# Kernel tuning notes

Measured on AMD Instinct MI355X. Metric: run time of the kernel, lower is better.

Reference implementation:

```python
import jax, jax.numpy as jnp
import numpy as np

B, T, D = 8, 1024, 1024
H, HD, KVH, R = 16, 64, 4, 256   # heads, head_dim, kv_heads, kv_lora_rank
K = 31                            # depthwise conv kernel
FF = 4 * D
EPS = 1e-5


def _ln(x, g, b):
    m = jnp.mean(x, -1, keepdims=True)
    v = jnp.mean((x - m) ** 2, -1, keepdims=True)
    return (x - m) * jax.lax.rsqrt(v + EPS) * g + b


def _rope_tables(seq, dim):
    inv = 1.0 / (10000.0 ** (np.arange(0, dim, 2, dtype=np.float32) / dim))
    t = np.arange(seq, dtype=np.float32)
    f = np.einsum('i,j->ij', t, inv)
    emb = np.concatenate([f, f], -1)
    return jnp.asarray(np.cos(emb)), jnp.asarray(np.sin(emb))


def _rope(x, cos, sin):
    # x: [B, h, T, HD]; cos/sin: [T, HD]
    x1, x2 = jnp.split(x, 2, axis=-1)
    return x * cos + jnp.concatenate([-x2, x1], -1) * sin


def setup_inputs() -> dict:
    key = jax.random.key(0)
    ks = iter(jax.random.split(key, 48))
    def w(shape, s=0.02):
        return jax.random.normal(next(ks), shape, jnp.float32) * s
    d = {}
    d['x'] = jax.random.normal(next(ks), (B, T, D), jnp.float32)
    d['ff1_ng'] = jnp.ones(D); d['ff1_nb'] = jnp.zeros(D)
    d['ff1_w1'] = w((D, FF)); d['ff1_b1'] = jnp.zeros(FF)
    d['ff1_w2'] = w((FF, D)); d['ff1_b2'] = jnp.zeros(D)
    d['attn_ng'] = jnp.ones(D); d['attn_nb'] = jnp.zeros(D)
    d['wq'] = w((D, H * HD)); d['wkva'] = w((D, R + HD))
    d['kvn_g'] = jnp.ones(R); d['kvn_b'] = jnp.zeros(R)
    d['wkvb'] = w((R, KVH * HD * 2)); d['wo'] = w((H * HD, D))
    d['conv_ng'] = jnp.ones(D); d['conv_nb'] = jnp.zeros(D)
    d['pw1_w'] = w((D, 2 * D)); d['pw1_b'] = jnp.zeros(2 * D)
    d['dw_w'] = w((D, 1, K)); d['dw_b'] = jnp.zeros(D)
    d['bn_g'] = jnp.ones(D); d['bn_b'] = jnp.zeros(D)
    d['bn_rm'] = jnp.zeros(D); d['bn_rv'] = jnp.ones(D)
    d['pw2_w'] = w((D, D)); d['pw2_b'] = jnp.zeros(D)
    d['ff2_ng'] = jnp.ones(D); d['ff2_nb'] = jnp.zeros(D)
    d['ff2_w1'] = w((D, FF)); d['ff2_b1'] = jnp.zeros(FF)
    d['ff2_w2'] = w((FF, D)); d['ff2_b2'] = jnp.zeros(D)
    d['fin_g'] = jnp.ones(D); d['fin_b'] = jnp.zeros(D)
    return d


def _ffn(x, ng, nb, w1, b1, w2, b2):
    h = jax.nn.silu(_ln(x, ng, nb) @ w1 + b1)
    return h @ w2 + b2


def _rmla(x, ng, nb, wq, wkva, kvn_g, kvn_b, wkvb, wo):
    h = _ln(x, ng, nb)
    q = (h @ wq).reshape(B, T, H, HD).transpose(0, 2, 1, 3)
    kva = h @ wkva                                  # [B,T,R+HD]; k_pe part unused (as in source)
    lat = _ln(kva[..., :R], kvn_g, kvn_b)
    kv = lat @ wkvb
    k = kv[..., :KVH * HD].reshape(B, T, KVH, HD).transpose(0, 2, 1, 3)
    v = kv[..., KVH * HD:].reshape(B, T, KVH, HD).transpose(0, 2, 1, 3)
    cos, sin = _rope_tables(T, HD)
    q = _rope(q, cos, sin)
    k = _rope(k, cos, sin)
    g = H // KVH
    k = jnp.repeat(k, g, axis=1)
    v = jnp.repeat(v, g, axis=1)
    s = jnp.einsum('bhqd,bhkd->bhqk', q, k) * (HD ** -0.5)
    a = jax.nn.softmax(s.astype(jnp.float32), axis=-1).astype(q.dtype)
    o = jnp.einsum('bhqk,bhkd->bhqd', a, v)
    o = o.transpose(0, 2, 1, 3).reshape(B, T, H * HD)
    return o @ wo


def _convmod(x, ng, nb, pw1_w, pw1_b, dw_w, dw_b, bn_g, bn_b, bn_rm, bn_rv, pw2_w, pw2_b):
    h = _ln(x, ng, nb)
    h = h @ pw1_w + pw1_b                           # [B,T,2D]
    a, gate = jnp.split(h, 2, axis=-1)
    h = a * jax.nn.sigmoid(gate)                    # GLU over channels
    h = h.transpose(0, 2, 1)                        # [B,D,T]
    h = jax.lax.conv_general_dilated(h, dw_w, (1,), [(K // 2, K // 2)],
                                     dimension_numbers=('NCH', 'OIH', 'NCH'),
                                     feature_group_count=D) + dw_b[None, :, None]
    h = (h - bn_rm[None, :, None]) * jax.lax.rsqrt(bn_rv[None, :, None] + EPS)
    h = h * bn_g[None, :, None] + bn_b[None, :, None]
    h = jax.nn.silu(h)
    h = h.transpose(0, 2, 1)                        # [B,T,D]
    return h @ pw2_w + pw2_b


def reference(x, ff1_ng, ff1_nb, ff1_w1, ff1_b1, ff1_w2, ff1_b2,
              attn_ng, attn_nb, wq, wkva, kvn_g, kvn_b, wkvb, wo,
              conv_ng, conv_nb, pw1_w, pw1_b, dw_w, dw_b, bn_g, bn_b, bn_rm, bn_rv, pw2_w, pw2_b,
              ff2_ng, ff2_nb, ff2_w1, ff2_b1, ff2_w2, ff2_b2, fin_g, fin_b):
    # Conformer block (macaron): half-FF, RMLA attention, gated depthwise conv, half-FF, final LN
    x = x + 0.5 * _ffn(x, ff1_ng, ff1_nb, ff1_w1, ff1_b1, ff1_w2, ff1_b2)
    x = x + _rmla(x, attn_ng, attn_nb, wq, wkva, kvn_g, kvn_b, wkvb, wo)
    x = x + _convmod(x, conv_ng, conv_nb, pw1_w, pw1_b, dw_w, dw_b, bn_g, bn_b, bn_rm, bn_rv, pw2_w, pw2_b)
    x = x + 0.5 * _ffn(x, ff2_ng, ff2_nb, ff2_w1, ff2_b1, ff2_w2, ff2_b2)
    return _ln(x, fin_g, fin_b)
```

## Files before the change

### kernel.cpp

```cpp
#include <hip/hip_runtime.h>
#include <stdint.h>

typedef unsigned short u16;
using bf16x8 = __attribute__((ext_vector_type(8))) __bf16;
using f32x4  = __attribute__((ext_vector_type(4))) float;

__device__ __forceinline__ u16 f2bf(float f) {
    uint32_t u = __float_as_uint(f);
    u += 0x7fffu + ((u >> 16) & 1u);
    return (u16)(u >> 16);
}
__device__ __forceinline__ float bf2f(u16 u) {
    return __uint_as_float(((uint32_t)u) << 16);
}
__device__ __forceinline__ void gload16(const void* g, void* l) {
    __builtin_amdgcn_global_load_lds(
        (__attribute__((address_space(1))) void*)(uintptr_t)g,
        (__attribute__((address_space(3))) void*)(uintptr_t)l,
        16, 0, 0);
}

template <int OUTF32>
__global__ __launch_bounds__(256) void ln_kernel(const float* __restrict__ in,
                                                 const float* __restrict__ g,
                                                 const float* __restrict__ b,
                                                 void* __restrict__ out, int D) {
    const int row = blockIdx.x;
    const int tid = threadIdx.x;
    const float* x = in + (size_t)row * D;
    const int nv = D >> 8;
    float v[4];
    float s1 = 0.f, s2 = 0.f;
    for (int i = 0; i < nv; ++i) {
        float t = x[tid + (i << 8)];
        v[i] = t; s1 += t; s2 += t * t;
    }
    for (int o = 1; o < 64; o <<= 1) {
        s1 += __shfl_xor(s1, o, 64);
        s2 += __shfl_xor(s2, o, 64);
    }
    __shared__ float r1[4], r2[4];
    const int w = tid >> 6;
    if ((tid & 63) == 0) { r1[w] = s1; r2[w] = s2; }
    __syncthreads();
    s1 = r1[0] + r1[1] + r1[2] + r1[3];
    s2 = r2[0] + r2[1] + r2[2] + r2[3];
    const float mean = s1 / (float)D;
    const float var  = s2 / (float)D - mean * mean;
    const float inv  = rsqrtf(var + 1e-5f);
    for (int i = 0; i < nv; ++i) {
        int c = tid + (i << 8);
        float y = (v[i] - mean) * inv * g[c] + b[c];
        if (OUTF32) ((float*)out)[(size_t)row * D + c] = y;
        else        ((u16*)out)[(size_t)row * D + c] = f2bf(y);
    }
}

template <int GLUPERM>
__global__ __launch_bounds__(256) void wconvert_t(const float* __restrict__ W,
                                                  u16* __restrict__ Wt,
                                                  int K, int N, int ldw) {
    __shared__ float tile[32][33];
    const int k0 = blockIdx.x * 32, n0 = blockIdx.y * 32;
    const int tx = threadIdx.x & 31, ty = threadIdx.x >> 5;
    const int csrc = GLUPERM ? ((tx & 1) * 1024 + (n0 >> 1) + (tx >> 1)) : (n0 + tx);
    for (int i = 0; i < 4; ++i)
        tile[ty + i * 8][tx] = W[(size_t)(k0 + ty + i * 8) * ldw + csrc];
    __syncthreads();
    for (int i = 0; i < 4; ++i)
        Wt[(size_t)(n0 + ty + i * 8) * K + k0 + tx] = f2bf(tile[tx][ty + i * 8]);
}

template <int EPI>
__global__ __launch_bounds__(256) void gemm_bf16(const u16* __restrict__ A,
                                                 const u16* __restrict__ Bt,
                                                 const float* __restrict__ bias,
                                                 const float* __restrict__ res,
                                                 float rscale,
                                                 void* __restrict__ outp,
                                                 int M, int N, int K, int nbx) {
    __shared__ u16 sA[128 * 64];
    __shared__ u16 sB[128 * 64];
    const int tid = threadIdx.x;
    const int lane = tid & 63;
    const int w = tid >> 6;
    const int wm = w >> 1, wn = w & 1;
    const int fr = lane & 15, fq = lane >> 4, frx = fr & 7;
    const int cpx = gridDim.x >> 3;
    const int lid = (blockIdx.x & 7) * cpx + (blockIdx.x >> 3);
    const int bn0 = (lid % nbx) * 128;
    const int bm0 = (lid / nbx) * 128;

    f32x4 acc[4][4] = {};

    const int lrow = lane >> 3;
    const int lslot = (lane & 7) ^ lrow;
    const u16* ga0 = A  + (size_t)(bm0 + w * 8 + lrow) * K + lslot * 8;
    const u16* gb0 = Bt + (size_t)(bn0 + w * 8 + lrow) * K + lslot * 8;
    u16* la0 = sA + w * 512;
    u16* lb0 = sB + w * 512;
    const size_t rstep32 = (size_t)32 * K;

    for (int kt = 0; kt < K; kt += 64) {
        __syncthreads();
#pragma unroll
        for (int i = 0; i < 4; ++i) {
            gload16(ga0 + kt + i * rstep32, la0 + i * 2048);
            gload16(gb0 + kt + i * rstep32, lb0 + i * 2048);
        }
        __syncthreads();
#pragma unroll
        for (int kk = 0; kk < 2; ++kk) {
            bf16x8 afr[4], bfr[4];
            const int sl = (((kk * 4 + fq) ^ frx) << 3);
#pragma unroll
            for (int i = 0; i < 4; ++i) {
                afr[i] = *(const bf16x8*)(sA + (wm * 64 + i * 16 + fr) * 64 + sl);
                bfr[i] = *(const bf16x8*)(sB + (wn * 64 + i * 16 + fr) * 64 + sl);
            }
#pragma unroll
            for (int mi = 0; mi < 4; ++mi)
#pragma unroll
                for (int ni = 0; ni < 4; ++ni)
                    acc[mi][ni] = __builtin_amdgcn_mfma_f32_16x16x32_bf16(
                        bfr[ni], afr[mi], acc[mi][ni], 0, 0, 0);
        }
    }

#pragma unroll
    for (int mi = 0; mi < 4; ++mi) {
        const int m = bm0 + wm * 64 + mi * 16 + fr;
#pragma unroll
        for (int ni = 0; ni < 4; ++ni) {
            const int n0 = bn0 + wn * 64 + ni * 16 + fq * 4;
            if (EPI == 0 || EPI == 1) {
                union { uint2 u2; u16 hh[4]; } ok;
#pragma unroll
                for (int r = 0; r < 4; ++r) {
                    float v = acc[mi][ni][r] + (bias ? bias[n0 + r] : 0.f);
                    if (EPI == 1) v = v / (1.f + __expf(-v));
                    ok.hh[r] = f2bf(v);
                }
                *(uint2*)((u16*)outp + (size_t)m * N + n0) = ok.u2;
            } else if (EPI == 2) {
                f32x4 v;
#pragma unroll
                for (int r = 0; r < 4; ++r)
                    v[r] = acc[mi][ni][r] + (bias ? bias[n0 + r] : 0.f);
                *(f32x4*)((float*)outp + (size_t)m * N + n0) = v;
            } else if (EPI == 3) {
                const f32x4 rv = *(const f32x4*)(res + (size_t)m * N + n0);
                f32x4 v;
#pragma unroll
                for (int r = 0; r < 4; ++r)
                    v[r] = rv[r] + rscale * (acc[mi][ni][r] + (bias ? bias[n0 + r] : 0.f));
                *(f32x4*)((float*)outp + (size_t)m * N + n0) = v;
            } else {
                float vv[4];
#pragma unroll
                for (int r = 0; r < 4; ++r) {
                    const int n = n0 + r;
                    vv[r] = acc[mi][ni][r] + bias[((n & 1) << 10) + (n >> 1)];
                }
                union { uint32_t u; u16 hh[2]; } ok;
                ok.hh[0] = f2bf(vv[0] / (1.f + __expf(-vv[1])));
                ok.hh[1] = f2bf(vv[2] / (1.f + __expf(-vv[3])));
                *(uint32_t*)((u16*)outp + (size_t)m * (N >> 1) + (n0 >> 1)) = ok.u;
            }
        }
    }
}

__global__ __launch_bounds__(256) void rope_tables_kernel(float* __restrict__ ct,
                                                          float* __restrict__ st) {
    const int i = blockIdx.x * 256 + threadIdx.x;
    const int t = i >> 5, j = i & 31;
    const float inv = powf(10000.f, -(float)j / 32.f);
    const float f = (float)t * inv;
    ct[i] = cosf(f);
    st[i] = sinf(f);
}

__global__ __launch_bounds__(256) void rope_kernel(u16* __restrict__ buf,
                                                   const float* __restrict__ ct,
                                                   const float* __restrict__ st,
                                                   int hmask, int hshift, int rstride,
                                                   float scale) {
    const int i = blockIdx.x * 256 + threadIdx.x;
    const int j = i & 31;
    const int hh = (i >> 5) & hmask;
    const int m = i >> (5 + hshift);
    const int t = m & 1023;
    u16* p = buf + (size_t)m * rstride + hh * 64 + j;
    const float c = ct[t * 32 + j], s = st[t * 32 + j];
    const float x1 = bf2f(p[0]), x2 = bf2f(p[32]);
    p[0]  = f2bf((x1 * c - x2 * s) * scale);
    p[32] = f2bf((x2 * c + x1 * s) * scale);
}

__global__ __launch_bounds__(256) void vtranspose_kernel(const u16* __restrict__ KV,
                                                         u16* __restrict__ Vt) {
    __shared__ u16 tile[32][33];
    const int t0 = blockIdx.x * 32, h0 = blockIdx.y * 32;
    const int bk = blockIdx.z;
    const int b = bk >> 2, kh = bk & 3;
    const int tx = threadIdx.x & 31, ty = threadIdx.x >> 5;
    for (int i = 0; i < 4; ++i)
        tile[ty + i * 8][tx] =
            KV[(size_t)(b * 1024 + t0 + ty + i * 8) * 512 + 256 + kh * 64 + h0 + tx];
    __syncthreads();
    for (int i = 0; i < 4; ++i)
        Vt[((size_t)bk * 64 + h0 + ty + i * 8) * 1024 + t0 + tx] = tile[tx][ty + i * 8];
}

__global__ __launch_bounds__(256) void attn_kernel(const u16* __restrict__ Q,
                                                   const u16* __restrict__ KV,
                                                   const u16* __restrict__ Vt,
                                                   u16* __restrict__ O) {
    __shared__ __align__(16) u16 sK[2][64 * 64];
    __shared__ __align__(16) u16 sV[2][64 * 64];
    __shared__ __align__(16) u16 sP[4][16 * 64];
    const int tid = threadIdx.x, lane = tid & 63, w = tid >> 6;
    const int fr = lane & 15, fq = lane >> 4, frx = fr & 7;
    const int bk = blockIdx.x, b = bk >> 2, kh = bk & 3;
    const int h = kh * 4 + w;
    const int q0 = blockIdx.y * 16;
    const int qrow = b * 1024 + q0 + fr;

    const int srow = w * 16 + (lane >> 3);
    const int sslot = (lane & 7) ^ ((lane >> 3) & 7);
    const u16* gK = KV + (size_t)(b * 1024 + srow) * 512 + kh * 64 + sslot * 8;
    const u16* gV = Vt + (size_t)((b * 4 + kh) * 64 + srow) * 1024 + sslot * 8;
    u16* dK = (u16*)sK + w * 16 * 64;
    u16* dV = (u16*)sV + w * 16 * 64;

    bf16x8 qf[2];
    qf[0] = *(const bf16x8*)(Q + (size_t)qrow * 1024 + h * 64 + fq * 8);
    qf[1] = *(const bf16x8*)(Q + (size_t)qrow * 1024 + h * 64 + 32 + fq * 8);

    f32x4 oacc[4] = {};
    float mrun = -1e30f, lrun = 0.f;
    u16* sPw = sP[w];

    gload16(gK, dK);
    gload16(gK + (size_t)8 * 512, dK + 8 * 64);
    gload16(gV, dV);
    gload16(gV + (size_t)8 * 1024, dV + 8 * 64);
    __syncthreads();

    int cur = 0;
    for (int t = 0; t < 16; ++t) {
        const int kv0 = t * 64;
        if (t < 15) {
            const int kn = kv0 + 64;
            const int nx = (cur ^ 1) * 4096;
            gload16(gK + (size_t)kn * 512,       dK + nx);
            gload16(gK + (size_t)(kn + 8) * 512, dK + nx + 8 * 64);
            gload16(gV + kn,                     dV + nx);
            gload16(gV + kn + (size_t)8 * 1024,  dV + nx + 8 * 64);
        }
        const u16* sKc = (u16*)sK + cur * 4096;
        const u16* sVc = (u16*)sV + cur * 4096;
        f32x4 sacc[4] = {};
#pragma unroll
        for (int ks = 0; ks < 2; ++ks)
#pragma unroll
            for (int nb = 0; nb < 4; ++nb) {
                const bf16x8 kf = *(const bf16x8*)(
                    sKc + (nb * 16 + fr) * 64 + (((ks * 4 + fq) ^ frx) << 3));
                sacc[nb] = __builtin_amdgcn_mfma_f32_16x16x32_bf16(kf, qf[ks], sacc[nb], 0, 0, 0);
            }
        float pm;
        {
            float a0 = fmaxf(fmaxf(sacc[0][0], sacc[0][1]), fmaxf(sacc[0][2], sacc[0][3]));
            float a1 = fmaxf(fmaxf(sacc[1][0], sacc[1][1]), fmaxf(sacc[1][2], sacc[1][3]));
            float a2 = fmaxf(fmaxf(sacc[2][0], sacc[2][1]), fmaxf(sacc[2][2], sacc[2][3]));
            float a3 = fmaxf(fmaxf(sacc[3][0], sacc[3][1]), fmaxf(sacc[3][2], sacc[3][3]));
            pm = fmaxf(fmaxf(a0, a1), fmaxf(a2, a3));
        }
        pm = fmaxf(pm, __shfl_xor(pm, 16, 64));
        pm = fmaxf(pm, __shfl_xor(pm, 32, 64));
        if (!__all(pm <= mrun + 8.f)) {
            const float mn = fmaxf(mrun, pm);
            const float al = __expf(mrun - mn);
            mrun = mn;
            lrun *= al;
#pragma unroll
            for (int f = 0; f < 4; ++f) {
                f32x4 tt = oacc[f];
#pragma unroll
                for (int r = 0; r < 4; ++r) tt[r] *= al;
                oacc[f] = tt;
            }
        }
        float rs = 0.f;
#pragma unroll
        for (int nb = 0; nb < 4; ++nb) {
            union { uint2 u2; u16 hh[4]; } pk;
#pragma unroll
            for (int r = 0; r < 4; ++r) {
                const float p = __expf(sacc[nb][r] - mrun);
                rs += p;
                pk.hh[r] = f2bf(p);
            }
            const int slotl = nb * 2 + (fq >> 1);
            *(uint2*)(sPw + fr * 64 + (((slotl ^ frx) << 3) | ((fq & 1) << 2))) = pk.u2;
        }
        rs += __shfl_xor(rs, 16, 64);
        rs += __shfl_xor(rs, 32, 64);
        lrun += rs;
        asm volatile("s_waitcnt lgkmcnt(0)" ::: "memory");
        __builtin_amdgcn_sched_barrier(0);
#pragma unroll
        for (int ks2 = 0; ks2 < 2; ++ks2) {
            const bf16x8 pf = *(const bf16x8*)(
                sPw + fr * 64 + (((ks2 * 4 + fq) ^ frx) << 3));
#pragma unroll
            for (int f = 0; f < 4; ++f) {
                const bf16x8 vf = *(const bf16x8*)(
                    sVc + (f * 16 + fr) * 64 + (((ks2 * 4 + fq) ^ frx) << 3));
                oacc[f] = __builtin_amdgcn_mfma_f32_16x16x32_bf16(vf, pf, oacc[f], 0, 0, 0);
            }
        }
        __syncthreads();
        cur ^= 1;
    }

    const float linv = 1.f / lrun;
#pragma unroll
    for (int f = 0; f < 4; ++f) {
        union { uint2 u2; u16 hh[4]; } ok;
#pragma unroll
        for (int r = 0; r < 4; ++r) ok.hh[r] = f2bf(oacc[f][r] * linv);
        *(uint2*)(O + (size_t)qrow * 1024 + h * 64 + f * 16 + fq * 4) = ok.u2;
    }
}

__global__ __launch_bounds__(256) void dwconv_kernel(const u16* __restrict__ G,
                                                     const float* __restrict__ wt,
                                                     const float* __restrict__ wb,
                                                     const float* __restrict__ bg,
                                                     const float* __restrict__ bb,
                                                     const float* __restrict__ rm,
                                                     const float* __restrict__ rv,
                                                     u16* __restrict__ out) {
    __shared__ u16 sg[38 * 256];
    const int tid = threadIdx.x;
    const int d = blockIdx.x * 256 + tid;
    const int t0 = blockIdx.y * 8;
    const int b = blockIdx.z;
    const size_t base = (size_t)b * 1024 * 1024 + d;
    for (int i = 0; i < 38; ++i) {
        const int t = t0 - 15 + i;
        sg[i * 256 + tid] = (t >= 0 && t < 1024) ? G[base + (size_t)t * 1024] : (u16)0;
    }
    __syncthreads();
    float wreg[31];
#pragma unroll
    for (int k = 0; k < 31; ++k) wreg[k] = wt[d * 31 + k];
    const float scale = bg[d] * rsqrtf(rv[d] + 1e-5f);
    const float addv = wb[d] - rm[d];
#pragma unroll
    for (int j = 0; j < 8; ++j) {
        float acc = 0.f;
#pragma unroll
        for (int k = 0; k < 31; ++k) acc += bf2f(sg[(j + k) * 256 + tid]) * wreg[k];
        float y = (acc + addv) * scale + bb[d];
        y = y / (1.f + __expf(-y));
        out[base + (size_t)(t0 + j) * 1024] = f2bf(y);
    }
}

extern "C" void kernel_launch(void* const* d_in, const int* in_sizes, int n_in,
                              void* d_out, int out_size, void* d_ws, size_t ws_size,
                              hipStream_t stream) {
    (void)in_sizes; (void)n_in; (void)out_size;

    const float* x       = (const float*)d_in[0];
    const float* ff1_ng  = (const float*)d_in[1];
    const float* ff1_nb  = (const float*)d_in[2];
    const float* ff1_w1  = (const float*)d_in[3];
    const float* ff1_b1  = (const float*)d_in[4];
    const float* ff1_w2  = (const float*)d_in[5];
    const float* ff1_b2  = (const float*)d_in[6];
    const float* attn_ng = (const float*)d_in[7];
    const float* attn_nb = (const float*)d_in[8];
    const float* wq      = (const float*)d_in[9];
    const float* wkva    = (const float*)d_in[10];
    const float* kvn_g   = (const float*)d_in[11];
    const float* kvn_b   = (const float*)d_in[12];
    const float* wkvb    = (const float*)d_in[13];
    const float* wo      = (const float*)d_in[14];
    const float* conv_ng = (const float*)d_in[15];
    const float* conv_nb = (const float*)d_in[16];
    const float* pw1_w   = (const float*)d_in[17];
    const float* pw1_b   = (const float*)d_in[18];
    const float* dw_w    = (const float*)d_in[19];
    const float* dw_b    = (const float*)d_in[20];
    const float* bn_g    = (const float*)d_in[21];
    const float* bn_b    = (const float*)d_in[22];
    const float* bn_rm   = (const float*)d_in[23];
    const float* bn_rv   = (const float*)d_in[24];
    const float* pw2_w   = (const float*)d_in[25];
    const float* pw2_b   = (const float*)d_in[26];
    const float* ff2_ng  = (const float*)d_in[27];
    const float* ff2_nb  = (const float*)d_in[28];
    const float* ff2_w1  = (const float*)d_in[29];
    const float* ff2_b1  = (const float*)d_in[30];
    const float* ff2_w2  = (const float*)d_in[31];
    const float* ff2_b2  = (const float*)d_in[32];
    const float* fin_g   = (const float*)d_in[33];
    const float* fin_b   = (const float*)d_in[34];

    const int M = 8192;
    char* ws = (char*)d_ws;
    size_t off = 0;
    auto alloc = [&](size_t bytes) {
        size_t o = off;
        off += (bytes + 255) & ~(size_t)255;
        return o;
    };
    const size_t o_ff1w1 = alloc((size_t)4096 * 1024 * 2);
    const size_t o_ff1w2 = alloc((size_t)1024 * 4096 * 2);
    const size_t o_wq    = alloc((size_t)1024 * 1024 * 2);
    const size_t o_wkva  = alloc((size_t)256 * 1024 * 2);
    const size_t o_wkvb  = alloc((size_t)512 * 256 * 2);
    const size_t o_wo    = alloc((size_t)1024 * 1024 * 2);
    const size_t o_pw1   = alloc((size_t)2048 * 1024 * 2);
    const size_t o_pw2   = alloc((size_t)1024 * 1024 * 2);
    const size_t o_ff2w1 = alloc((size_t)4096 * 1024 * 2);
    const size_t o_ff2w2 = alloc((size_t)1024 * 4096 * 2);
    const size_t o_ctab  = alloc((size_t)1024 * 32 * 4);
    const size_t o_stab  = alloc((size_t)1024 * 32 * 4);
    const size_t o_xres  = alloc((size_t)M * 1024 * 4);
    const size_t o_ln    = alloc((size_t)M * 1024 * 2);
    const size_t o_bufa  = alloc((size_t)64 * 1024 * 1024);
    if (ws_size < off) return;

    u16* BUFA = (u16*)(ws + o_bufa);
    u16* Qb    = BUFA;
    u16* KVb   = (u16*)((char*)BUFA + (16u << 20));
    float* KVA = (float*)((char*)BUFA + (24u << 20));
    u16* LAT   = (u16*)((char*)BUFA + (32u << 20));
    u16* VT    = (u16*)((char*)BUFA + (36u << 20));
    u16* OB    = (u16*)((char*)BUFA + (40u << 20));
    u16* PW1G  = BUFA;
    u16* CONVO = (u16*)((char*)BUFA + (16u << 20));
    u16* HID   = BUFA;

    u16* WT_FF1W1 = (u16*)(ws + o_ff1w1);
    u16* WT_FF1W2 = (u16*)(ws + o_ff1w2);
    u16* WT_WQ    = (u16*)(ws + o_wq);
    u16* WT_WKVA  = (u16*)(ws + o_wkva);
    u16* WT_WKVB  = (u16*)(ws + o_wkvb);
    u16* WT_WO    = (u16*)(ws + o_wo);
    u16* WT_PW1   = (u16*)(ws + o_pw1);
    u16* WT_PW2   = (u16*)(ws + o_pw2);
    u16* WT_FF2W1 = (u16*)(ws + o_ff2w1);
    u16* WT_FF2W2 = (u16*)(ws + o_ff2w2);
    float* CT = (float*)(ws + o_ctab);
    float* ST = (float*)(ws + o_stab);
    float* XR = (float*)(ws + o_xres);
    u16* LNB  = (u16*)(ws + o_ln);

    wconvert_t<0><<<dim3(32, 128), 256, 0, stream>>>(ff1_w1, WT_FF1W1, 1024, 4096, 4096);
    wconvert_t<0><<<dim3(128, 32), 256, 0, stream>>>(ff1_w2, WT_FF1W2, 4096, 1024, 1024);
    wconvert_t<0><<<dim3(32, 32),  256, 0, stream>>>(wq,     WT_WQ,    1024, 1024, 1024);
    wconvert_t<0><<<dim3(32, 8),   256, 0, stream>>>(wkva,   WT_WKVA,  1024, 256,  320);
    wconvert_t<0><<<dim3(8, 16),   256, 0, stream>>>(wkvb,   WT_WKVB,  256,  512,  512);
    wconvert_t<0><<<dim3(32, 32),  256, 0, stream>>>(wo,     WT_WO,    1024, 1024, 1024);
    wconvert_t<1><<<dim3(32, 64),  256, 0, stream>>>(pw1_w,  WT_PW1,   1024, 2048, 2048);
    wconvert_t<0><<<dim3(32, 32),  256, 0, stream>>>(pw2_w,  WT_PW2,   1024, 1024, 1024);
    wconvert_t<0><<<dim3(32, 128), 256, 0, stream>>>(ff2_w1, WT_FF2W1, 1024, 4096, 4096);
    wconvert_t<0><<<dim3(128, 32), 256, 0, stream>>>(ff2_w2, WT_FF2W2, 4096, 1024, 1024);
    rope_tables_kernel<<<128, 256, 0, stream>>>(CT, ST);

    ln_kernel<0><<<M, 256, 0, stream>>>(x, ff1_ng, ff1_nb, LNB, 1024);
    gemm_bf16<1><<<2048, 256, 0, stream>>>(LNB, WT_FF1W1, ff1_b1, nullptr, 0.f, HID, M, 4096, 1024, 32);
    gemm_bf16<3><<<512, 256, 0, stream>>>(HID, WT_FF1W2, ff1_b2, x, 0.5f, XR, M, 1024, 4096, 8);

    ln_kernel<0><<<M, 256, 0, stream>>>(XR, attn_ng, attn_nb, LNB, 1024);
    gemm_bf16<0><<<512, 256, 0, stream>>>(LNB, WT_WQ, nullptr, nullptr, 0.f, Qb, M, 1024, 1024, 8);
    gemm_bf16<2><<<128, 256, 0, stream>>>(LNB, WT_WKVA, nullptr, nullptr, 0.f, KVA, M, 256, 1024, 2);
    ln_kernel<0><<<M, 256, 0, stream>>>(KVA, kvn_g, kvn_b, LAT, 256);
    gemm_bf16<0><<<256, 256, 0, stream>>>(LAT, WT_WKVB, nullptr, nullptr, 0.f, KVb, M, 512, 256, 4);
    rope_kernel<<<16384, 256, 0, stream>>>(Qb, CT, ST, 15, 4, 1024, 0.125f);
    rope_kernel<<<4096, 256, 0, stream>>>(KVb, CT, ST, 3, 2, 512, 1.0f);
    vtranspose_kernel<<<dim3(32, 2, 32), 256, 0, stream>>>(KVb, VT);
    attn_kernel<<<dim3(32, 64), 256, 0, stream>>>(Qb, KVb, VT, OB);
    gemm_bf16<3><<<512, 256, 0, stream>>>(OB, WT_WO, nullptr, XR, 1.f, XR, M, 1024, 1024, 8);

    ln_kernel<0><<<M, 256, 0, stream>>>(XR, conv_ng, conv_nb, LNB, 1024);
    gemm_bf16<4><<<1024, 256, 0, stream>>>(LNB, WT_PW1, pw1_b, nullptr, 0.f, PW1G, M, 2048, 1024, 16);
    dwconv_kernel<<<dim3(4, 128, 8), 256, 0, stream>>>(PW1G, dw_w, dw_b, bn_g, bn_b, bn_rm, bn_rv, CONVO);
    gemm_bf16<3><<<512, 256, 0, stream>>>(CONVO, WT_PW2, pw2_b, XR, 1.f, XR, M, 1024, 1024, 8);

    ln_kernel<0><<<M, 256, 0, stream>>>(XR, ff2_ng, ff2_nb, LNB, 1024);
    gemm_bf16<1><<<2048, 256, 0, stream>>>(LNB, WT_FF2W1, ff2_b1, nullptr, 0.f, HID, M, 4096, 1024, 32);
    gemm_bf16<3><<<512, 256, 0, stream>>>(HID, WT_FF2W2, ff2_b2, XR, 0.5f, XR, M, 1024, 4096, 8);

    ln_kernel<1><<<M, 256, 0, stream>>>(XR, fin_g, fin_b, d_out, 1024);
}
```

Baseline: 809.9 us.

## Add 256-row double-buffered 512-thread GEMM for large projections

Adds a new GEMM kernel with 256-row tiles, 8 waves, double-buffered LDS fed by async global-to-LDS loads, explicit waitcnt and barrier pipelining, and MFMA priority raising. The large FFN, Q, output, and pointwise-conv projections are routed to it, while the old kernel keeps only the small epilogue variants. Larger tiles raise data reuse per LDS load and the pipelining overlaps loads with MFMA work. The cost is higher LDS use (up to 128KB per block) and register pressure, which limit occupancy, plus fewer blocks for the smaller GEMMs.

```diff
diff --git a/kernel.cpp b/kernel.cpp
--- a/kernel.cpp
+++ b/kernel.cpp
@@ -69,6 +69,147 @@
     __syncthreads();
     for (int i = 0; i < 4; ++i)
         Wt[(size_t)(n0 + ty + i * 8) * K + k0 + tx] = f2bf(tile[tx][ty + i * 8]);
+}
+
+template <int EPI, int WM>
+__global__ __launch_bounds__(512, 2) void gemm256(const u16* __restrict__ A,
+                                                  const u16* __restrict__ Bt,
+                                                  const float* __restrict__ bias,
+                                                  const float* __restrict__ res,
+                                                  float rscale,
+                                                  void* __restrict__ outp,
+                                                  int M, int N, int K, int nbx) {
+    constexpr int WN = 8 / WM;
+    constexpr int BN = WN * 64;
+    constexpr int FM = 16 / WM;
+    __shared__ u16 sA[2][256 * 64];
+    __shared__ u16 sB[2][BN * 64];
+    const int tid = threadIdx.x, lane = tid & 63, w = tid >> 6;
+    const int wm = w / WN, wn = w % WN;
+    const int fr = lane & 15, fq = lane >> 4, frx = fr & 7;
+    const int cpx = gridDim.x >> 3;
+    const int lid = (blockIdx.x & 7) * cpx + (blockIdx.x >> 3);
+    const int bn0 = (lid % nbx) * BN;
+    const int bm0 = (lid / nbx) * 256;
+
+    f32x4 acc[FM][4] = {};
+
+    const int lrow = lane >> 3;
+    const int lslot = (lane & 7) ^ (lrow & 7);
+    const u16* ga = A  + (size_t)(bm0 + w * 8 + lrow) * K + lslot * 8;
+    const u16* gb = Bt + (size_t)(bn0 + w * 8 + lrow) * K + lslot * 8;
+    const size_t rs64 = (size_t)64 * K;
+    const int lbase = w * 8 * 64;
+
+    const int NK = K >> 6;
+
+#define STAGE(bufi, kt)                                                        \
+    {                                                                          \
+        _Pragma("unroll")                                                      \
+        for (int i = 0; i < 4; ++i)                                            \
+            gload16(ga + (kt) + i * rs64, &sA[bufi][lbase + i * 4096]);        \
+        _Pragma("unroll")                                                      \
+        for (int i = 0; i < BN / 64; ++i)                                      \
+            gload16(gb + (kt) + i * rs64, &sB[bufi][lbase + i * 4096]);        \
+    }
+
+    STAGE(0, 0)
+    STAGE(1, 64)
+    if constexpr (WM == 2) asm volatile("s_waitcnt vmcnt(8)" ::: "memory");
+    else                   asm volatile("s_waitcnt vmcnt(6)" ::: "memory");
+    __builtin_amdgcn_sched_barrier(0);
+    __builtin_amdgcn_s_barrier();
+
+    const int arow0 = wm * (256 / WM) + fr;
+    const int brow0 = wn * 64 + fr;
+
+    for (int s = 0; s < NK; ++s) {
+        const int buf = s & 1;
+        bf16x8 afr[FM], bfr[4];
+#pragma unroll
+        for (int mi = 0; mi < FM; ++mi)
+            afr[mi] = *(const bf16x8*)(&sA[buf][(arow0 + mi * 16) * 64 + ((fq ^ frx) << 3)]);
+#pragma unroll
+        for (int ni = 0; ni < 4; ++ni)
+            bfr[ni] = *(const bf16x8*)(&sB[buf][(brow0 + ni * 16) * 64 + ((fq ^ frx) << 3)]);
+        asm volatile("s_waitcnt lgkmcnt(0)" ::: "memory");
+        __builtin_amdgcn_sched_barrier(0);
+        __builtin_amdgcn_s_setprio(1);
+#pragma unroll
+        for (int mi = 0; mi < FM; ++mi)
+#pragma unroll
+            for (int ni = 0; ni < 4; ++ni)
+                acc[mi][ni] = __builtin_amdgcn_mfma_f32_16x16x32_bf16(
+                    bfr[ni], afr[mi], acc[mi][ni], 0, 0, 0);
+        __builtin_amdgcn_s_setprio(0);
+#pragma unroll
+        for (int mi = 0; mi < FM; ++mi)
+            afr[mi] = *(const bf16x8*)(&sA[buf][(arow0 + mi * 16) * 64 + (((4 + fq) ^ frx) << 3)]);
+#pragma unroll
+        for (int ni = 0; ni < 4; ++ni)
+            bfr[ni] = *(const bf16x8*)(&sB[buf][(brow0 + ni * 16) * 64 + (((4 + fq) ^ frx) << 3)]);
+        asm volatile("s_waitcnt lgkmcnt(0)" ::: "memory");
+        __builtin_amdgcn_sched_barrier(0);
+        __builtin_amdgcn_s_barrier();
+        if (s + 2 < NK) {
+            STAGE(buf, (s + 2) << 6)
+        }
+        __builtin_amdgcn_sched_barrier(0);
+        __builtin_amdgcn_s_setprio(1);
+#pragma unroll
+        for (int mi = 0; mi < FM; ++mi)
+#pragma unroll
+            for (int ni = 0; ni < 4; ++ni)
+                acc[mi][ni] = __builtin_amdgcn_mfma_f32_16x16x32_bf16(
+                    bfr[ni], afr[mi], acc[mi][ni], 0, 0, 0);
+        __builtin_amdgcn_s_setprio(0);
+        if (s + 2 < NK) {
+            if constexpr (WM == 2) asm volatile("s_waitcnt vmcnt(8)" ::: "memory");
+            else                   asm volatile("s_waitcnt vmcnt(6)" ::: "memory");
+        } else {
+            asm volatile("s_waitcnt vmcnt(0)" ::: "memory");
+        }
+        __builtin_amdgcn_sched_barrier(0);
+        __builtin_amdgcn_s_barrier();
+    }
+
+#pragma unroll
+    for (int mi = 0; mi < FM; ++mi) {
+        const int m = bm0 + wm * (256 / WM) + mi * 16 + fr;
+#pragma unroll
+        for (int ni = 0; ni < 4; ++ni) {
+            const int n0 = bn0 + wn * 64 + ni * 16 + fq * 4;
+            if (EPI == 0 || EPI == 1) {
+                union { uint2 u2; u16 hh[4]; } ok;
+#pragma unroll
+                for (int r = 0; r < 4; ++r) {
+                    float v = acc[mi][ni][r] + (bias ? bias[n0 + r] : 0.f);
+                    if (EPI == 1) v = v / (1.f + __expf(-v));
+                    ok.hh[r] = f2bf(v);
+                }
+                *(uint2*)((u16*)outp + (size_t)m * N + n0) = ok.u2;
+            } else if (EPI == 3) {
+                const f32x4 rv = *(const f32x4*)(res + (size_t)m * N + n0);
+                f32x4 v;
+#pragma unroll
+                for (int r = 0; r < 4; ++r)
+                    v[r] = rv[r] + rscale * (acc[mi][ni][r] + (bias ? bias[n0 + r] : 0.f));
+                *(f32x4*)((float*)outp + (size_t)m * N + n0) = v;
+            } else {
+                float vv[4];
+#pragma unroll
+                for (int r = 0; r < 4; ++r) {
+                    const int n = n0 + r;
+                    vv[r] = acc[mi][ni][r] + bias[((n & 1) << 10) + (n >> 1)];
+                }
+                union { uint32_t u; u16 hh[2]; } ok;
+                ok.hh[0] = f2bf(vv[0] / (1.f + __expf(-vv[1])));
+                ok.hh[1] = f2bf(vv[2] / (1.f + __expf(-vv[3])));
+                *(uint32_t*)((u16*)outp + (size_t)m * (N >> 1) + (n0 >> 1)) = ok.u;
+            }
+        }
+    }
+#undef STAGE
 }
 
 template <int EPI>
@@ -133,39 +274,18 @@
 #pragma unroll
         for (int ni = 0; ni < 4; ++ni) {
             const int n0 = bn0 + wn * 64 + ni * 16 + fq * 4;
-            if (EPI == 0 || EPI == 1) {
+            if (EPI == 0) {
                 union { uint2 u2; u16 hh[4]; } ok;
 #pragma unroll
-                for (int r = 0; r < 4; ++r) {
-                    float v = acc[mi][ni][r] + (bias ? bias[n0 + r] : 0.f);
-                    if (EPI == 1) v = v / (1.f + __expf(-v));
-                    ok.hh[r] = f2bf(v);
-                }
+                for (int r = 0; r < 4; ++r)
+                    ok.hh[r] = f2bf(acc[mi][ni][r] + (bias ? bias[n0 + r] : 0.f));
                 *(uint2*)((u16*)outp + (size_t)m * N + n0) = ok.u2;
-            } else if (EPI == 2) {
+            } else {
                 f32x4 v;
 #pragma unroll
                 for (int r = 0; r < 4; ++r)
                     v[r] = acc[mi][ni][r] + (bias ? bias[n0 + r] : 0.f);
                 *(f32x4*)((float*)outp + (size_t)m * N + n0) = v;
-            } else if (EPI == 3) {
-                const f32x4 rv = *(const f32x4*)(res + (size_t)m * N + n0);
-                f32x4 v;
-#pragma unroll
-                for (int r = 0; r < 4; ++r)
-                    v[r] = rv[r] + rscale * (acc[mi][ni][r] + (bias ? bias[n0 + r] : 0.f));
-                *(f32x4*)((float*)outp + (size_t)m * N + n0) = v;
-            } else {
-                float vv[4];
-#pragma unroll
-                for (int r = 0; r < 4; ++r) {
-                    const int n = n0 + r;
-                    vv[r] = acc[mi][ni][r] + bias[((n & 1) << 10) + (n >> 1)];
-                }
-                union { uint32_t u; u16 hh[2]; } ok;
-                ok.hh[0] = f2bf(vv[0] / (1.f + __expf(-vv[1])));
-                ok.hh[1] = f2bf(vv[2] / (1.f + __expf(-vv[3])));
-                *(uint32_t*)((u16*)outp + (size_t)m * (N >> 1) + (n0 >> 1)) = ok.u;
             }
         }
     }
@@ -476,11 +596,11 @@
     rope_tables_kernel<<<128, 256, 0, stream>>>(CT, ST);
 
     ln_kernel<0><<<M, 256, 0, stream>>>(x, ff1_ng, ff1_nb, LNB, 1024);
-    gemm_bf16<1><<<2048, 256, 0, stream>>>(LNB, WT_FF1W1, ff1_b1, nullptr, 0.f, HID, M, 4096, 1024, 32);
-    gemm_bf16<3><<<512, 256, 0, stream>>>(HID, WT_FF1W2, ff1_b2, x, 0.5f, XR, M, 1024, 4096, 8);
+    gemm256<1, 2><<<512, 512, 0, stream>>>(LNB, WT_FF1W1, ff1_b1, nullptr, 0.f, HID, M, 4096, 1024, 16);
+    gemm256<3, 4><<<256, 512, 0, stream>>>(HID, WT_FF1W2, ff1_b2, x, 0.5f, XR, M, 1024, 4096, 8);
 
     ln_kernel<0><<<M, 256, 0, stream>>>(XR, attn_ng, attn_nb, LNB, 1024);
-    gemm_bf16<0><<<512, 256, 0, stream>>>(LNB, WT_WQ, nullptr, nullptr, 0.f, Qb, M, 1024, 1024, 8);
+    gemm256<0, 4><<<256, 512, 0, stream>>>(LNB, WT_WQ, nullptr, nullptr, 0.f, Qb, M, 1024, 1024, 8);
     gemm_bf16<2><<<128, 256, 0, stream>>>(LNB, WT_WKVA, nullptr, nullptr, 0.f, KVA, M, 256, 1024, 2);
     ln_kernel<0><<<M, 256, 0, stream>>>(KVA, kvn_g, kvn_b, LAT, 256);
     gemm_bf16<0><<<256, 256, 0, stream>>>(LAT, WT_WKVB, nullptr, nullptr, 0.f, KVb, M, 512, 256, 4);
@@ -488,16 +608,16 @@
     rope_kernel<<<4096, 256, 0, stream>>>(KVb, CT, ST, 3, 2, 512, 1.0f);
     vtranspose_kernel<<<dim3(32, 2, 32), 256, 0, stream>>>(KVb, VT);
     attn_kernel<<<dim3(32, 64), 256, 0, stream>>>(Qb, KVb, VT, OB);
-    gemm_bf16<3><<<512, 256, 0, stream>>>(OB, WT_WO, nullptr, XR, 1.f, XR, M, 1024, 1024, 8);
+    gemm256<3, 4><<<256, 512, 0, stream>>>(OB, WT_WO, nullptr, XR, 1.f, XR, M, 1024, 1024, 8);
 
     ln_kernel<0><<<M, 256, 0, stream>>>(XR, conv_ng, conv_nb, LNB, 1024);
-    gemm_bf16<4><<<1024, 256, 0, stream>>>(LNB, WT_PW1, pw1_b, nullptr, 0.f, PW1G, M, 2048, 1024, 16);
+    gemm256<4, 2><<<256, 512, 0, stream>>>(LNB, WT_PW1, pw1_b, nullptr, 0.f, PW1G, M, 2048, 1024, 8);
     dwconv_kernel<<<dim3(4, 128, 8), 256, 0, stream>>>(PW1G, dw_w, dw_b, bn_g, bn_b, bn_rm, bn_rv, CONVO);
-    gemm_bf16<3><<<512, 256, 0, stream>>>(CONVO, WT_PW2, pw2_b, XR, 1.f, XR, M, 1024, 1024, 8);
+    gemm256<3, 4><<<256, 512, 0, stream>>>(CONVO, WT_PW2, pw2_b, XR, 1.f, XR, M, 1024, 1024, 8);
 
     ln_kernel<0><<<M, 256, 0, stream>>>(XR, ff2_ng, ff2_nb, LNB, 1024);
-    gemm_bf16<1><<<2048, 256, 0, stream>>>(LNB, WT_FF2W1, ff2_b1, nullptr, 0.f, HID, M, 4096, 1024, 32);
-    gemm_bf16<3><<<512, 256, 0, stream>>>(HID, WT_FF2W2, ff2_b2, XR, 0.5f, XR, M, 1024, 4096, 8);
+    gemm256<1, 2><<<512, 512, 0, stream>>>(LNB, WT_FF2W1, ff2_b1, nullptr, 0.f, HID, M, 4096, 1024, 16);
+    gemm256<3, 4><<<256, 512, 0, stream>>>(HID, WT_FF2W2, ff2_b2, XR, 0.5f, XR, M, 1024, 4096, 8);
 
     ln_kernel<1><<<M, 256, 0, stream>>>(XR, fin_g, fin_b, d_out, 1024);
 }
```

New measurement: 756.3 us. 6.6% less time.

## Add 8-wave pipelined bf16 GEMM with larger tiles for large projections

Applied to the files above, without the earlier changes.

Introduces a 512-thread GEMM kernel with 256x256 or 256x128 tiles, double-buffered LDS split into K halves, swizzled LDS reads, explicit vmcnt waits, barriers and setprio, so that global-to-LDS loads overlap with MFMA work. It replaces the old 128x128 GEMM for the FFN, Q, output projection and pointwise conv projections, and the old kernel keeps only the small epilogues. The aim is more data reuse per tile and better load/compute overlap. In exchange it raises register and LDS pressure, and the hand-tuned wait counts are fragile.

```diff
diff --git a/kernel.cpp b/kernel.cpp
--- a/kernel.cpp
+++ b/kernel.cpp
@@ -69,6 +69,228 @@
     __syncthreads();
     for (int i = 0; i < 4; ++i)
         Wt[(size_t)(n0 + ty + i * 8) * K + k0 + tx] = f2bf(tile[tx][ty + i * 8]);
+}
+
+template <int EPI, int WM>
+__global__ __launch_bounds__(512, 2) void gemm8p(const u16* __restrict__ A,
+                                                 const u16* __restrict__ Bt,
+                                                 const float* __restrict__ bias,
+                                                 const float* __restrict__ res,
+                                                 float rscale,
+                                                 void* __restrict__ outp,
+                                                 int M, int N, int K, int nbx) {
+    constexpr int WN = 8 / WM;
+    constexpr int BN = (WM == 2) ? 256 : 128;
+    constexpr int FM = (WM == 2) ? 8 : 4;
+    constexpr int LB = BN / 128;
+    __shared__ u16 sA[2][2][128 * 64];
+    __shared__ u16 sB[2][2][(BN / 2) * 64];
+
+    const int tid = threadIdx.x, lane = tid & 63, w = tid >> 6;
+    const int wm = w / WN, wn = w % WN;
+    const int fr = lane & 15, fq = lane >> 4;
+    const int cpx = gridDim.x >> 3;
+    const int lid = (blockIdx.x & 7) * cpx + (blockIdx.x >> 3);
+    const int bn0 = (lid % nbx) * BN;
+    const int bm0 = (lid / nbx) * 256;
+
+    const int rdbase = (fr >> 1) * 64 + ((((((fr & 1) << 2) | fq)) ^ (fr >> 1)) << 3);
+    const int s_l = (lane & 7) ^ (lane >> 3);
+    const int rowoff_l = 2 * (lane >> 3) + (s_l >> 2);
+    const int koff_l = (s_l & 3) << 3;
+
+    f32x4 acc[FM][4] = {};
+    const int NK = K >> 6;
+    const int arow = wm * (256 / WM);
+    const int brow = wn * 64;
+
+#define STAGE_A(bufi, kh, t)                                                    \
+    {                                                                           \
+        _Pragma("unroll")                                                       \
+        for (int c = 0; c < 2; ++c)                                             \
+            gload16(A + (size_t)(bm0 + (c * 8 + w) * 16 + rowoff_l) * K         \
+                        + ((t) << 6) + (kh) * 32 + koff_l,                      \
+                    &sA[bufi][kh][(c * 8 + w) * 512]);                          \
+    }
+#define STAGE_B(bufi, kh, t)                                                    \
+    {                                                                           \
+        _Pragma("unroll")                                                       \
+        for (int c = 0; c < LB; ++c)                                            \
+            gload16(Bt + (size_t)(bn0 + (c * 8 + w) * 16 + rowoff_l) * K        \
+                        + ((t) << 6) + (kh) * 32 + koff_l,                      \
+                    &sB[bufi][kh][(c * 8 + w) * 512]);                          \
+    }
+#define RD_A(dst, bufi, kh, r0)                                                 \
+    dst = *(const bf16x8*)(&sA[bufi][kh][((r0) >> 1) * 64 + rdbase]);
+#define RD_B(dst, bufi, kh, r0)                                                 \
+    dst = *(const bf16x8*)(&sB[bufi][kh][((r0) >> 1) * 64 + rdbase]);
+#define BARRIER() __builtin_amdgcn_s_barrier()
+#define LGK0()                                                                  \
+    asm volatile("s_waitcnt lgkmcnt(0)" ::: "memory");                          \
+    __builtin_amdgcn_sched_barrier(0)
+#define SB() __builtin_amdgcn_sched_barrier(0)
+
+    STAGE_A(0, 0, 0) STAGE_B(0, 0, 0)
+    STAGE_A(0, 1, 0) STAGE_B(0, 1, 0)
+    STAGE_A(1, 0, 1) STAGE_B(1, 0, 1)
+    if constexpr (WM == 2) { asm volatile("s_waitcnt vmcnt(8)" ::: "memory"); }
+    else                   { asm volatile("s_waitcnt vmcnt(6)" ::: "memory"); }
+    SB();
+    BARRIER();
+
+    for (int s = 0; s < NK; ++s) {
+        const int buf = s & 1;
+        bf16x8 afr[4], bfr[4];
+        if constexpr (WM == 2) {
+#pragma unroll
+            for (int i = 0; i < 4; ++i) { RD_B(bfr[i], buf, 0, brow + i * 16) }
+#pragma unroll
+            for (int i = 0; i < 4; ++i) { RD_A(afr[i], buf, 0, arow + i * 16) }
+            if (s + 1 < NK) STAGE_A(buf ^ 1, 1, s + 1)
+            BARRIER(); LGK0();
+            __builtin_amdgcn_s_setprio(1);
+#pragma unroll
+            for (int i = 0; i < 4; ++i)
+#pragma unroll
+                for (int j = 0; j < 4; ++j)
+                    acc[i][j] = __builtin_amdgcn_mfma_f32_16x16x32_bf16(
+                        bfr[j], afr[i], acc[i][j], 0, 0, 0);
+            __builtin_amdgcn_s_setprio(0);
+            BARRIER();
+#pragma unroll
+            for (int i = 0; i < 4; ++i) { RD_A(afr[i], buf, 0, arow + 64 + i * 16) }
+            if (s + 1 < NK) STAGE_B(buf ^ 1, 1, s + 1)
+            BARRIER(); LGK0();
+            __builtin_amdgcn_s_setprio(1);
+#pragma unroll
+            for (int i = 0; i < 4; ++i)
+#pragma unroll
+                for (int j = 0; j < 4; ++j)
+                    acc[4 + i][j] = __builtin_amdgcn_mfma_f32_16x16x32_bf16(
+                        bfr[j], afr[i], acc[4 + i][j], 0, 0, 0);
+            __builtin_amdgcn_s_setprio(0);
+            if (s + 1 < NK) { asm volatile("s_waitcnt vmcnt(8)" ::: "memory"); }
+            else            { asm volatile("s_waitcnt vmcnt(0)" ::: "memory"); }
+            SB();
+            BARRIER();
+#pragma unroll
+            for (int i = 0; i < 4; ++i) { RD_B(bfr[i], buf, 1, brow + i * 16) }
+#pragma unroll
+            for (int i = 0; i < 4; ++i) { RD_A(afr[i], buf, 1, arow + i * 16) }
+            if (s + 2 < NK) STAGE_A(buf, 0, s + 2)
+            BARRIER(); LGK0();
+            __builtin_amdgcn_s_setprio(1);
+#pragma unroll
+            for (int i = 0; i < 4; ++i)
+#pragma unroll
+                for (int j = 0; j < 4; ++j)
+                    acc[i][j] = __builtin_amdgcn_mfma_f32_16x16x32_bf16(
+                        bfr[j], afr[i], acc[i][j], 0, 0, 0);
+            __builtin_amdgcn_s_setprio(0);
+            BARRIER();
+#pragma unroll
+            for (int i = 0; i < 4; ++i) { RD_A(afr[i], buf, 1, arow + 64 + i * 16) }
+            if (s + 2 < NK) STAGE_B(buf, 0, s + 2)
+            BARRIER(); LGK0();
+            __builtin_amdgcn_s_setprio(1);
+#pragma unroll
+            for (int i = 0; i < 4; ++i)
+#pragma unroll
+                for (int j = 0; j < 4; ++j)
+                    acc[4 + i][j] = __builtin_amdgcn_mfma_f32_16x16x32_bf16(
+                        bfr[j], afr[i], acc[4 + i][j], 0, 0, 0);
+            __builtin_amdgcn_s_setprio(0);
+            if (s + 1 < NK) {
+                if (s + 2 < NK) { asm volatile("s_waitcnt vmcnt(8)" ::: "memory"); }
+                else            { asm volatile("s_waitcnt vmcnt(4)" ::: "memory"); }
+                SB();
+            }
+            BARRIER();
+        } else {
+#pragma unroll
+            for (int i = 0; i < 4; ++i) { RD_B(bfr[i], buf, 0, brow + i * 16) }
+#pragma unroll
+            for (int i = 0; i < 4; ++i) { RD_A(afr[i], buf, 0, arow + i * 16) }
+            if (s + 1 < NK) { STAGE_A(buf ^ 1, 1, s + 1) STAGE_B(buf ^ 1, 1, s + 1) }
+            BARRIER(); LGK0();
+            __builtin_amdgcn_s_setprio(1);
+#pragma unroll
+            for (int i = 0; i < 4; ++i)
+#pragma unroll
+                for (int j = 0; j < 4; ++j)
+                    acc[i][j] = __builtin_amdgcn_mfma_f32_16x16x32_bf16(
+                        bfr[j], afr[i], acc[i][j], 0, 0, 0);
+            __builtin_amdgcn_s_setprio(0);
+            if (s + 1 < NK) { asm volatile("s_waitcnt vmcnt(6)" ::: "memory"); }
+            else            { asm volatile("s_waitcnt vmcnt(0)" ::: "memory"); }
+            SB();
+            BARRIER();
+#pragma unroll
+            for (int i = 0; i < 4; ++i) { RD_B(bfr[i], buf, 1, brow + i * 16) }
+#pragma unroll
+            for (int i = 0; i < 4; ++i) { RD_A(afr[i], buf, 1, arow + i * 16) }
+            if (s + 2 < NK) { STAGE_A(buf, 0, s + 2) STAGE_B(buf, 0, s + 2) }
+            BARRIER(); LGK0();
+            __builtin_amdgcn_s_setprio(1);
+#pragma unroll
+            for (int i = 0; i < 4; ++i)
+#pragma unroll
+                for (int j = 0; j < 4; ++j)
+                    acc[i][j] = __builtin_amdgcn_mfma_f32_16x16x32_bf16(
+                        bfr[j], afr[i], acc[i][j], 0, 0, 0);
+            __builtin_amdgcn_s_setprio(0);
+            if (s + 1 < NK) {
+                if (s + 2 < NK) { asm volatile("s_waitcnt vmcnt(6)" ::: "memory"); }
+                else            { asm volatile("s_waitcnt vmcnt(3)" ::: "memory"); }
+                SB();
+            }
+            BARRIER();
+        }
+    }
+
+#pragma unroll
+    for (int mi = 0; mi < FM; ++mi) {
+        const int m = bm0 + wm * (256 / WM) + mi * 16 + fr;
+#pragma unroll
+        for (int ni = 0; ni < 4; ++ni) {
+            const int n0 = bn0 + wn * 64 + ni * 16 + fq * 4;
+            if (EPI == 0 || EPI == 1) {
+                union { uint2 u2; u16 hh[4]; } ok;
+#pragma unroll
+                for (int r = 0; r < 4; ++r) {
+                    float v = acc[mi][ni][r] + (bias ? bias[n0 + r] : 0.f);
+                    if (EPI == 1) v = v / (1.f + __expf(-v));
+                    ok.hh[r] = f2bf(v);
+                }
+                *(uint2*)((u16*)outp + (size_t)m * N + n0) = ok.u2;
+            } else if (EPI == 3) {
+                const f32x4 rv = *(const f32x4*)(res + (size_t)m * N + n0);
+                f32x4 v;
+#pragma unroll
+                for (int r = 0; r < 4; ++r)
+                    v[r] = rv[r] + rscale * (acc[mi][ni][r] + (bias ? bias[n0 + r] : 0.f));
+                *(f32x4*)((float*)outp + (size_t)m * N + n0) = v;
+            } else {
+                float vv[4];
+#pragma unroll
+                for (int r = 0; r < 4; ++r) {
+                    const int n = n0 + r;
+                    vv[r] = acc[mi][ni][r] + bias[((n & 1) << 10) + (n >> 1)];
+                }
+                union { uint32_t u; u16 hh[2]; } ok;
+                ok.hh[0] = f2bf(vv[0] / (1.f + __expf(-vv[1])));
+                ok.hh[1] = f2bf(vv[2] / (1.f + __expf(-vv[3])));
+                *(uint32_t*)((u16*)outp + (size_t)m * (N >> 1) + (n0 >> 1)) = ok.u;
+            }
+        }
+    }
+#undef STAGE_A
+#undef STAGE_B
+#undef RD_A
+#undef RD_B
+#undef BARRIER
+#undef LGK0
+#undef SB
 }
 
 template <int EPI>
@@ -133,39 +355,18 @@
 #pragma unroll
         for (int ni = 0; ni < 4; ++ni) {
             const int n0 = bn0 + wn * 64 + ni * 16 + fq * 4;
-            if (EPI == 0 || EPI == 1) {
+            if (EPI == 0) {
                 union { uint2 u2; u16 hh[4]; } ok;
 #pragma unroll
-                for (int r = 0; r < 4; ++r) {
-                    float v = acc[mi][ni][r] + (bias ? bias[n0 + r] : 0.f);
-                    if (EPI == 1) v = v / (1.f + __expf(-v));
-                    ok.hh[r] = f2bf(v);
-                }
+                for (int r = 0; r < 4; ++r)
+                    ok.hh[r] = f2bf(acc[mi][ni][r] + (bias ? bias[n0 + r] : 0.f));
                 *(uint2*)((u16*)outp + (size_t)m * N + n0) = ok.u2;
-            } else if (EPI == 2) {
+            } else {
                 f32x4 v;
 #pragma unroll
                 for (int r = 0; r < 4; ++r)
                     v[r] = acc[mi][ni][r] + (bias ? bias[n0 + r] : 0.f);
                 *(f32x4*)((float*)outp + (size_t)m * N + n0) = v;
-            } else if (EPI == 3) {
-                const f32x4 rv = *(const f32x4*)(res + (size_t)m * N + n0);
-                f32x4 v;
-#pragma unroll
-                for (int r = 0; r < 4; ++r)
-                    v[r] = rv[r] + rscale * (acc[mi][ni][r] + (bias ? bias[n0 + r] : 0.f));
-                *(f32x4*)((float*)outp + (size_t)m * N + n0) = v;
-            } else {
-                float vv[4];
-#pragma unroll
-                for (int r = 0; r < 4; ++r) {
-                    const int n = n0 + r;
-                    vv[r] = acc[mi][ni][r] + bias[((n & 1) << 10) + (n >> 1)];
-                }
-                union { uint32_t u; u16 hh[2]; } ok;
-                ok.hh[0] = f2bf(vv[0] / (1.f + __expf(-vv[1])));
-                ok.hh[1] = f2bf(vv[2] / (1.f + __expf(-vv[3])));
-                *(uint32_t*)((u16*)outp + (size_t)m * (N >> 1) + (n0 >> 1)) = ok.u;
             }
         }
     }
@@ -476,11 +677,11 @@
     rope_tables_kernel<<<128, 256, 0, stream>>>(CT, ST);
 
     ln_kernel<0><<<M, 256, 0, stream>>>(x, ff1_ng, ff1_nb, LNB, 1024);
-    gemm_bf16<1><<<2048, 256, 0, stream>>>(LNB, WT_FF1W1, ff1_b1, nullptr, 0.f, HID, M, 4096, 1024, 32);
-    gemm_bf16<3><<<512, 256, 0, stream>>>(HID, WT_FF1W2, ff1_b2, x, 0.5f, XR, M, 1024, 4096, 8);
+    gemm8p<1, 2><<<512, 512, 0, stream>>>(LNB, WT_FF1W1, ff1_b1, nullptr, 0.f, HID, M, 4096, 1024, 16);
+    gemm8p<3, 4><<<256, 512, 0, stream>>>(HID, WT_FF1W2, ff1_b2, x, 0.5f, XR, M, 1024, 4096, 8);
 
     ln_kernel<0><<<M, 256, 0, stream>>>(XR, attn_ng, attn_nb, LNB, 1024);
-    gemm_bf16<0><<<512, 256, 0, stream>>>(LNB, WT_WQ, nullptr, nullptr, 0.f, Qb, M, 1024, 1024, 8);
+    gemm8p<0, 4><<<256, 512, 0, stream>>>(LNB, WT_WQ, nullptr, nullptr, 0.f, Qb, M, 1024, 1024, 8);
     gemm_bf16<2><<<128, 256, 0, stream>>>(LNB, WT_WKVA, nullptr, nullptr, 0.f, KVA, M, 256, 1024, 2);
     ln_kernel<0><<<M, 256, 0, stream>>>(KVA, kvn_g, kvn_b, LAT, 256);
     gemm_bf16<0><<<256, 256, 0, stream>>>(LAT, WT_WKVB, nullptr, nullptr, 0.f, KVb, M, 512, 256, 4);
@@ -488,16 +689,16 @@
     rope_kernel<<<4096, 256, 0, stream>>>(KVb, CT, ST, 3, 2, 512, 1.0f);
     vtranspose_kernel<<<dim3(32, 2, 32), 256, 0, stream>>>(KVb, VT);
     attn_kernel<<<dim3(32, 64), 256, 0, stream>>>(Qb, KVb, VT, OB);
-    gemm_bf16<3><<<512, 256, 0, stream>>>(OB, WT_WO, nullptr, XR, 1.f, XR, M, 1024, 1024, 8);
+    gemm8p<3, 4><<<256, 512, 0, stream>>>(OB, WT_WO, nullptr, XR, 1.f, XR, M, 1024, 1024, 8);
 
     ln_kernel<0><<<M, 256, 0, stream>>>(XR, conv_ng, conv_nb, LNB, 1024);
-    gemm_bf16<4><<<1024, 256, 0, stream>>>(LNB, WT_PW1, pw1_b, nullptr, 0.f, PW1G, M, 2048, 1024, 16);
+    gemm8p<4, 2><<<256, 512, 0, stream>>>(LNB, WT_PW1, pw1_b, nullptr, 0.f, PW1G, M, 2048, 1024, 8);
     dwconv_kernel<<<dim3(4, 128, 8), 256, 0, stream>>>(PW1G, dw_w, dw_b, bn_g, bn_b, bn_rm, bn_rv, CONVO);
-    gemm_bf16<3><<<512, 256, 0, stream>>>(CONVO, WT_PW2, pw2_b, XR, 1.f, XR, M, 1024, 1024, 8);
+    gemm8p<3, 4><<<256, 512, 0, stream>>>(CONVO, WT_PW2, pw2_b, XR, 1.f, XR, M, 1024, 1024, 8);
 
     ln_kernel<0><<<M, 256, 0, stream>>>(XR, ff2_ng, ff2_nb, LNB, 1024);
-    gemm_bf16<1><<<2048, 256, 0, stream>>>(LNB, WT_FF2W1, ff2_b1, nullptr, 0.f, HID, M, 4096, 1024, 32);
-    gemm_bf16<3><<<512, 256, 0, stream>>>(HID, WT_FF2W2, ff2_b2, XR, 0.5f, XR, M, 1024, 4096, 8);
+    gemm8p<1, 2><<<512, 512, 0, stream>>>(LNB, WT_FF2W1, ff2_b1, nullptr, 0.f, HID, M, 4096, 1024, 16);
+    gemm8p<3, 4><<<256, 512, 0, stream>>>(HID, WT_FF2W2, ff2_b2, XR, 0.5f, XR, M, 1024, 4096, 8);
 
     ln_kernel<1><<<M, 256, 0, stream>>>(XR, fin_g, fin_b, d_out, 1024);
 }
```

Result: faster. 784.2 us (-3.2%).
